# Performance work log

Hardware: AMD Instinct MI355X
Metric: run time of the kernel (lower is better)

Reference implementation:

```python
import jax, jax.numpy as jnp
import numpy as np

B, T, C = 2, 2048, 1024
H, D = 16, 64
EPS = 1e-6


def _layernorm(x, gamma, beta):
    # Faithful to the torch module: uses unbiased std (Bessel) and divides by (std + eps).
    mean = x.mean(-1, keepdims=True)
    std = jnp.sqrt(jnp.sum((x - mean) ** 2, axis=-1, keepdims=True) / (x.shape[-1] - 1))
    return gamma * (x - mean) / (std + EPS) + beta


def setup_inputs() -> dict:
    key = jax.random.key(0)
    ks = jax.random.split(key, 9)
    s = lambda fan_in: 1.0 / np.sqrt(fan_in)
    return {
        "x": jax.random.normal(ks[0], (B, T, C), dtype=jnp.float32),
        "qkv_w": jax.random.uniform(ks[1], (3 * C, C), jnp.float32, -s(C), s(C)),
        "proj_w": jax.random.uniform(ks[2], (C, C), jnp.float32, -s(C), s(C)),
        "proj_b": jax.random.uniform(ks[3], (C,), jnp.float32, -s(C), s(C)),
        "l1_w": jax.random.uniform(ks[4], (4 * C, C), jnp.float32, -s(C), s(C)),
        "l1_b": jax.random.uniform(ks[5], (4 * C,), jnp.float32, -s(C), s(C)),
        "l3_w": jax.random.uniform(ks[6], (C, 4 * C), jnp.float32, -s(4 * C), s(4 * C)),
        "l3_b": jax.random.uniform(ks[7], (C,), jnp.float32, -s(4 * C), s(4 * C)),
        "ln1_g": jnp.ones((C,), jnp.float32),
        "ln1_b": jnp.zeros((C,), jnp.float32),
        "ln2_g": jnp.ones((C,), jnp.float32),
        "ln2_b": jnp.zeros((C,), jnp.float32),
    }


def _attention(x, qkv_w, proj_w, proj_b):
    Bx, Tx, Cx = x.shape
    qkv = x @ qkv_w.T                      # [B,T,3C]
    q, k, v = jnp.split(qkv, 3, axis=-1)
    q = q.reshape(Bx, Tx, H, D)
    k = k.reshape(Bx, Tx, H, D)
    v = v.reshape(Bx, Tx, H, D)
    scores = jnp.einsum("bthd,bshd->bhts", q, k) * (D ** -0.5)  # [B,H,T,T]
    causal = jnp.tril(jnp.ones((Tx, Tx), dtype=bool))
    scores = jnp.where(causal, scores, -jnp.inf)
    attn = jax.nn.softmax(scores, axis=-1)
    out = jnp.einsum("bhts,bshd->bthd", attn, v).reshape(Bx, Tx, Cx)
    return out @ proj_w.T + proj_b


def _mlp(x, l1_w, l1_b, l3_w, l3_b):
    h = jax.nn.relu(x @ l1_w.T + l1_b)     # [B,T,4C]
    return h @ l3_w.T + l3_b


def reference(x, qkv_w, proj_w, proj_b, l1_w, l1_b, l3_w, l3_b, ln1_g, ln1_b, ln2_g, ln2_b):
    # Dropout is identity in eval mode.
    x1 = x + _attention(_layernorm(x, ln1_g, ln1_b), qkv_w, proj_w, proj_b)
    x2 = x1 + _mlp(_layernorm(x1, ln2_g, ln2_b), l1_w, l1_b, l3_w, l3_b)
    return x2
```

## Files before the change

kernel.cpp:

```cpp
#include <hip/hip_runtime.h>

typedef unsigned short u16;
typedef short short8 __attribute__((ext_vector_type(8)));
typedef float floatx4 __attribute__((ext_vector_type(4)));

#define TT 2048
#define CC 1024
#define QSCALE 0.1803368801111244f
#define MFIX 32.0f

__device__ __forceinline__ u16 f2bf(float f) {
  return (u16)((__float_as_uint(f) + 0x8000u) >> 16);
}

__device__ __forceinline__ unsigned int pk2bf(float a, float b) {
  unsigned int ua = __float_as_uint(a) + 0x8000u;
  unsigned int ub = __float_as_uint(b) + 0x8000u;
  return __builtin_amdgcn_perm(ub, ua, 0x07060302u);
}

__device__ __forceinline__ void glds16(const u16* g, u16* l) {
  __builtin_amdgcn_global_load_lds((const __attribute__((address_space(1))) void*)g,
                                   (__attribute__((address_space(3))) void*)l, 16, 0, 0);
}

__device__ __forceinline__ void ln_body(const float* __restrict__ x,
                                        const float* __restrict__ g,
                                        const float* __restrict__ b,
                                        u16* __restrict__ out, int row, int tid) {
  const float4* xr = (const float4*)(x + (size_t)row * CC);
  float4 v = xr[tid];
  float s = v.x + v.y + v.z + v.w;
  float sq = v.x * v.x + v.y * v.y + v.z * v.z + v.w * v.w;
#pragma unroll
  for (int off = 1; off < 64; off <<= 1) {
    s += __shfl_xor(s, off);
    sq += __shfl_xor(sq, off);
  }
  __shared__ float ss[4], ssq[4];
  int wave = tid >> 6;
  if ((tid & 63) == 0) { ss[wave] = s; ssq[wave] = sq; }
  __syncthreads();
  s = ss[0] + ss[1] + ss[2] + ss[3];
  sq = ssq[0] + ssq[1] + ssq[2] + ssq[3];
  float mean = s * (1.0f / CC);
  float var = (sq - (float)CC * mean * mean) * (1.0f / (CC - 1));
  float inv = 1.0f / (sqrtf(fmaxf(var, 0.0f)) + 1e-6f);
  float4 gv = ((const float4*)g)[tid];
  float4 bv = ((const float4*)b)[tid];
  ushort4 o;
  o.x = f2bf(gv.x * (v.x - mean) * inv + bv.x);
  o.y = f2bf(gv.y * (v.y - mean) * inv + bv.y);
  o.z = f2bf(gv.z * (v.z - mean) * inv + bv.z);
  o.w = f2bf(gv.w * (v.w - mean) * inv + bv.w);
  ((ushort4*)(out + (size_t)row * CC))[tid] = o;
}

__global__ __launch_bounds__(256) void cvt_ln_kernel(const float* __restrict__ w0,
                                                     const float* __restrict__ w1,
                                                     const float* __restrict__ w2,
                                                     const float* __restrict__ w3,
                                                     const float* __restrict__ x,
                                                     const float* __restrict__ lg,
                                                     const float* __restrict__ lb,
                                                     u16* __restrict__ o0,
                                                     u16* __restrict__ o1,
                                                     u16* __restrict__ o2,
                                                     u16* __restrict__ o3,
                                                     u16* __restrict__ oln) {
  int blk = blockIdx.x;
  if (blk >= 12288) {
    ln_body(x, lg, lb, oln, blk - 12288, threadIdx.x);
    return;
  }
  const float* in;
  u16* out;
  int base;
  if (blk < 3072)      { in = w0; out = o0; base = 0; }
  else if (blk < 4096) { in = w1; out = o1; base = 3072; }
  else if (blk < 8192) { in = w2; out = o2; base = 4096; }
  else                 { in = w3; out = o3; base = 8192; }
  int i = (blk - base) * 256 + threadIdx.x;
  float4 v = ((const float4*)in)[i];
  ushort4 o;
  o.x = f2bf(v.x); o.y = f2bf(v.y); o.z = f2bf(v.z); o.w = f2bf(v.w);
  ((ushort4*)out)[i] = o;
}

__global__ __launch_bounds__(256) void ln_kernel(const float* __restrict__ x,
                                                 const float* __restrict__ g,
                                                 const float* __restrict__ b,
                                                 u16* __restrict__ out) {
  ln_body(x, g, b, out, blockIdx.x, threadIdx.x);
}


#define STGP(st, g_)                                                      \
  glds16(gsrc + (size_t)(st) * 32 + (size_t)(g_) * 16 * K,                \
         &lds[(st) & 3][ldst + (g_) * 512])

#define BODY(t, VM)                                                       \
  {                                                                       \
    asm volatile("s_waitcnt vmcnt(" #VM ")" ::: "memory");                \
    __builtin_amdgcn_s_barrier();                                         \
    asm volatile("" ::: "memory");                                        \
    const u16* Ls = &lds[(t) & 3][0];                                     \
    bool stg_ = (t) + 3 < nst;                                            \
    if (stg_) {                                                           \
      _Pragma("unroll") for (int g_ = 0; g_ < GPP; g_++) STGP((t) + 3, g_); \
    }                                                                     \
    short8 bf[NJ];                                                        \
    _Pragma("unroll") for (int j_ = 0; j_ < NJ; j_++)                     \
        bf[j_] = *(const short8*)(Ls + bOff[j_]);                         \
    short8 a0_ = *(const short8*)(Ls + aOff[0]);                          \
    short8 a1_ = *(const short8*)(Ls + aOff[1]);                          \
    __builtin_amdgcn_s_setprio(1);                                        \
    _Pragma("unroll") for (int j_ = 0; j_ < NJ; j_++)                     \
        acc[0][j_] = __builtin_amdgcn_mfma_f32_16x16x32_bf16(a0_, bf[j_], acc[0][j_], 0, 0, 0); \
    _Pragma("unroll") for (int j_ = 0; j_ < NJ; j_++)                     \
        acc[1][j_] = __builtin_amdgcn_mfma_f32_16x16x32_bf16(a1_, bf[j_], acc[1][j_], 0, 0, 0); \
    __builtin_amdgcn_s_setprio(0);                                        \
    _Pragma("unroll") for (int ph_ = 1; ph_ < NPH; ph_++) {               \
      short8 c0_ = *(const short8*)(Ls + aOff[2 * ph_]);                  \
      short8 c1_ = *(const short8*)(Ls + aOff[2 * ph_ + 1]);              \
      if (stg_) {                                                         \
        _Pragma("unroll") for (int g_ = 0; g_ < GPP; g_++)                \
            STGP((t) + 3, ph_ * GPP + g_);                                \
      }                                                                   \
      __builtin_amdgcn_s_barrier();                                       \
      asm volatile("" ::: "memory");                                      \
      __builtin_amdgcn_s_setprio(1);                                      \
      _Pragma("unroll") for (int j_ = 0; j_ < NJ; j_++)                   \
          acc[2 * ph_][j_] = __builtin_amdgcn_mfma_f32_16x16x32_bf16(c0_, bf[j_], acc[2 * ph_][j_], 0, 0, 0); \
      _Pragma("unroll") for (int j_ = 0; j_ < NJ; j_++)                   \
          acc[2 * ph_ + 1][j_] = __builtin_amdgcn_mfma_f32_16x16x32_bf16(c1_, bf[j_], acc[2 * ph_ + 1][j_], 0, 0, 0); \
      __builtin_amdgcn_s_setprio(0);                                      \
    }                                                                     \
  }

template <int BM, int BN, int NWM, int NWN, int MODE>
__global__ __launch_bounds__(64 * NWM * NWN, 2) void gemmp(
    const u16* __restrict__ A, const u16* __restrict__ W,
    const float* __restrict__ bias, const float* __restrict__ resid,
    float* __restrict__ outf, u16* __restrict__ outb,
    int M, int N, int K) {
  constexpr int NW = NWM * NWN;
  constexpr int MI = BM / NWM / 16;
  constexpr int NJ = BN / NWN / 16;
  constexpr int ROWS = BM + BN;
  constexpr int NPH = MI / 2;
  constexpr int GPP = 4 / NPH;
  static_assert(ROWS / NW == 64, "each wave stages 64 rows");
  __shared__ u16 lds[4][ROWS * 32];

  const int tid = threadIdx.x;
  const int w = tid >> 6, lane = tid & 63;
  const int l15 = lane & 15, quad = lane >> 4;
  const int wm = (w / NWN) * (MI * 16);
  const int wn = (w % NWN) * (NJ * 16);
  const int tm = blockIdx.x * BM, tn = blockIdx.y * BN;

  const int srow = lane >> 2;
  const int xk = (lane & 3) ^ ((lane >> 4) & 3);
  const int wrow = w * 64;
  const u16* rowbase = (wrow < BM) ? (A + (size_t)(tm + wrow) * K)
                                   : (W + (size_t)(tn + wrow - BM) * K);
  const u16* gsrc = rowbase + (size_t)srow * K + xk * 8;
  const int ldst = wrow * 32;

  const int rx = (l15 >> 2) & 3;
  int aOff[MI], bOff[NJ];
#pragma unroll
  for (int m = 0; m < MI; m++) aOff[m] = (wm + m * 16 + l15) * 32 + ((quad ^ rx) * 8);
#pragma unroll
  for (int j = 0; j < NJ; j++) bOff[j] = (BM + wn + j * 16 + l15) * 32 + ((quad ^ rx) * 8);

  floatx4 acc[MI][NJ];
#pragma unroll
  for (int m = 0; m < MI; m++)
#pragma unroll
    for (int j = 0; j < NJ; j++) acc[m][j] = (floatx4){0.f, 0.f, 0.f, 0.f};

  const int nst = K >> 5;

#pragma unroll
  for (int st = 0; st < 3; st++)
#pragma unroll
    for (int g = 0; g < 4; g++) STGP(st, g);

#pragma unroll 4
  for (int t = 0; t < nst - 2; ++t) BODY(t, 8);
  BODY(nst - 2, 4);
  BODY(nst - 1, 0);

  float bb[NJ];
#pragma unroll
  for (int j = 0; j < NJ; j++)
    bb[j] = (MODE == 1 || MODE == 2) ? bias[tn + wn + j * 16 + l15] : 0.0f;
#pragma unroll
  for (int m = 0; m < MI; m++) {
    int row0 = tm + wm + m * 16 + quad * 4;
#pragma unroll
    for (int j = 0; j < NJ; j++) {
      int col = tn + wn + j * 16 + l15;
#pragma unroll
      for (int r = 0; r < 4; r++) {
        float v = acc[m][j][r];
        size_t idx = (size_t)(row0 + r) * N + col;
        if (MODE == 0) {
          if (col < 1024) v *= QSCALE;
          outb[idx] = f2bf(v);
        } else if (MODE == 1) {
          outf[idx] = v + bb[j] + resid[idx];
        } else {
          outb[idx] = f2bf(fmaxf(v + bb[j], 0.0f));
        }
      }
    }
  }
}

#undef STGP
#undef BODY

__global__ __launch_bounds__(256) void flash_kernel(const u16* __restrict__ qkv,
                                                    u16* __restrict__ attn) {
  int bid = blockIdx.x;
  int qt = 31 - (bid >> 5);
  int bh = bid & 31;
  int b = bh >> 4, h = bh & 15;
  int tid = threadIdx.x, w = tid >> 6, lane = tid & 63;
  int l15 = lane & 15, quad = lane >> 4;

  __shared__ u16 k_lds[128 * 64];
  __shared__ u16 vt_lds[64 * 136];
  __shared__ u16 p_lds[4][16 * 136];

  int qbase = qt * 64 + w * 16;
  const u16* qp = qkv + (size_t)(b * TT + qbase + l15) * 3072 + h * 64;
  short8 qf0 = *(const short8*)(qp + quad * 8);
  short8 qf1 = *(const short8*)(qp + 32 + quad * 8);

  float l_i = 0.0f;
  floatx4 accO[4];
#pragma unroll
  for (int jf = 0; jf < 4; jf++) accO[jf] = (floatx4){0.f, 0.f, 0.f, 0.f};

  int rsub = lane >> 3;
  int cg = (lane & 7) ^ rsub;
  const u16* Kg = qkv + (size_t)(b * TT + w * 32 + rsub) * 3072 + 1024 + h * 64 + cg * 8;
  u16* kL = k_lds + w * 32 * 64;
  int s4 = (tid & 31) * 4;
  int dg = (tid >> 5) * 8;
  const u16* Vg = qkv + (size_t)(b * TT + s4) * 3072 + 2048 + h * 64 + dg;

  int x = l15 & 7;
  int kOff[8];
#pragma unroll
  for (int i = 0; i < 8; i++) kOff[i] = (i * 16 + l15) * 64 + ((quad ^ x) * 8);
  int pRd = l15 * 136 + quad * 8;

  int nt = (qt + 2) >> 1;
  for (int kt = 0; kt < nt; kt++) {
    int s0 = kt * 128;
    size_t soff = (size_t)s0 * 3072;
    uint4 R0 = *(const uint4*)(Vg + soff);
    uint4 R1 = *(const uint4*)(Vg + soff + 3072);
    uint4 R2 = *(const uint4*)(Vg + soff + 6144);
    uint4 R3 = *(const uint4*)(Vg + soff + 9216);
    __syncthreads();
#pragma unroll
    for (int is = 0; is < 4; is++) glds16(Kg + soff + (size_t)is * 8 * 3072, kL + is * 512);
    {
      unsigned int a0[4] = {R0.x, R0.y, R0.z, R0.w};
      unsigned int a1[4] = {R1.x, R1.y, R1.z, R1.w};
      unsigned int a2[4] = {R2.x, R2.y, R2.z, R2.w};
      unsigned int a3[4] = {R3.x, R3.y, R3.z, R3.w};
#pragma unroll
      for (int p = 0; p < 4; p++) {
        uint2 ev, od;
        ev.x = __builtin_amdgcn_perm(a1[p], a0[p], 0x05040100u);
        ev.y = __builtin_amdgcn_perm(a3[p], a2[p], 0x05040100u);
        od.x = __builtin_amdgcn_perm(a1[p], a0[p], 0x07060302u);
        od.y = __builtin_amdgcn_perm(a3[p], a2[p], 0x07060302u);
        *(uint2*)(vt_lds + (dg + 2 * p) * 136 + s4) = ev;
        *(uint2*)(vt_lds + (dg + 2 * p + 1) * 136 + s4) = od;
      }
    }
    __syncthreads();

    floatx4 st[8];
#pragma unroll
    for (int i = 0; i < 8; i++) st[i] = (floatx4){0.f, 0.f, 0.f, 0.f};
#pragma unroll
    for (int i = 0; i < 8; i++) {
      short8 kf0 = *(const short8*)(k_lds + kOff[i]);
      short8 kf1 = *(const short8*)(k_lds + (kOff[i] ^ 32));
      st[i] = __builtin_amdgcn_mfma_f32_16x16x32_bf16(kf0, qf0, st[i], 0, 0, 0);
      st[i] = __builtin_amdgcn_mfma_f32_16x16x32_bf16(kf1, qf1, st[i], 0, 0, 0);
    }

    if (s0 + 127 > qbase) {
      int mg = qbase + l15;
#pragma unroll
      for (int i = 0; i < 8; i++)
#pragma unroll
        for (int r = 0; r < 4; r++) {
          int s = s0 + i * 16 + quad * 4 + r;
          if (s > mg) st[i][r] = -3.0e38f;
        }
    }

    float ts = 0.0f;
#pragma unroll
    for (int i = 0; i < 8; i++)
#pragma unroll
      for (int r = 0; r < 4; r++) {
        float p = __builtin_amdgcn_exp2f(st[i][r] - MFIX);
        st[i][r] = p;
        ts += p;
      }
    ts += __shfl_xor(ts, 16);
    ts += __shfl_xor(ts, 32);
    l_i += ts;

#pragma unroll
    for (int i = 0; i < 8; i++) {
      uint2 pk;
      pk.x = pk2bf(st[i][0], st[i][1]);
      pk.y = pk2bf(st[i][2], st[i][3]);
      *(uint2*)(p_lds[w] + l15 * 136 + i * 16 + quad * 4) = pk;
    }

    short8 pf[4];
#pragma unroll
    for (int c = 0; c < 4; c++) pf[c] = *(const short8*)(p_lds[w] + pRd + c * 32);
#pragma unroll
    for (int jf = 0; jf < 4; jf++) {
      int vOff = (jf * 16 + l15) * 136 + quad * 8;
#pragma unroll
      for (int c = 0; c < 4; c++) {
        short8 vf = *(const short8*)(vt_lds + vOff + c * 32);
        accO[jf] = __builtin_amdgcn_mfma_f32_16x16x32_bf16(pf[c], vf, accO[jf], 0, 0, 0);
      }
    }
  }

  float invl = 1.0f / l_i;
  float iR[4];
#pragma unroll
  for (int r = 0; r < 4; r++) iR[r] = __shfl(invl, quad * 4 + r);
  int orow = b * TT + qbase + quad * 4;
#pragma unroll
  for (int r = 0; r < 4; r++) {
    u16* op = attn + (size_t)(orow + r) * CC + h * 64 + l15;
#pragma unroll
    for (int jf = 0; jf < 4; jf++) op[jf * 16] = f2bf(accO[jf][r] * iR[r]);
  }
}

extern "C" void kernel_launch(void* const* d_in, const int* in_sizes, int n_in,
                              void* d_out, int out_size, void* d_ws, size_t ws_size,
                              hipStream_t stream) {
  const float* x      = (const float*)d_in[0];
  const float* qkv_w  = (const float*)d_in[1];
  const float* proj_w = (const float*)d_in[2];
  const float* proj_b = (const float*)d_in[3];
  const float* l1_w   = (const float*)d_in[4];
  const float* l1_b   = (const float*)d_in[5];
  const float* l3_w   = (const float*)d_in[6];
  const float* l3_b   = (const float*)d_in[7];
  const float* ln1_g  = (const float*)d_in[8];
  const float* ln1_b  = (const float*)d_in[9];
  const float* ln2_g  = (const float*)d_in[10];
  const float* ln2_b  = (const float*)d_in[11];
  float* out = (float*)d_out;
  char* ws = (char*)d_ws;

  u16* w_qkv  = (u16*)(ws + 0);
  u16* w_proj = (u16*)(ws + 6291456);
  u16* w_l1   = (u16*)(ws + 8388608);
  u16* w_l3   = (u16*)(ws + 16777216);
  u16* lnb    = (u16*)(ws + 25165824);
  u16* qkvb   = (u16*)(ws + 33554432);
  u16* attnb  = (u16*)(ws + 58720256);
  float* x1   = (float*)(ws + 67108864);
  u16* hb     = (u16*)(ws + 83886080);

  cvt_ln_kernel<<<16384, 256, 0, stream>>>(qkv_w, proj_w, l1_w, l3_w, x, ln1_g, ln1_b,
                                           w_qkv, w_proj, w_l1, w_l3, lnb);
  gemmp<256, 256, 2, 4, 0><<<dim3(16, 12), 512, 0, stream>>>(
      lnb, w_qkv, nullptr, nullptr, nullptr, qkvb, 4096, 3072, 1024);
  flash_kernel<<<1024, 256, 0, stream>>>(qkvb, attnb);
  gemmp<128, 128, 2, 2, 1><<<dim3(32, 8), 256, 0, stream>>>(
      attnb, w_proj, proj_b, x, x1, nullptr, 4096, 1024, 1024);
  ln_kernel<<<4096, 256, 0, stream>>>(x1, ln2_g, ln2_b, lnb);
  gemmp<256, 256, 2, 4, 2><<<dim3(16, 16), 512, 0, stream>>>(
      lnb, w_l1, l1_b, nullptr, nullptr, hb, 4096, 4096, 1024);
  gemmp<128, 128, 2, 2, 1><<<dim3(32, 8), 256, 0, stream>>>(
      hb, w_l3, l3_b, x1, out, nullptr, 4096, 1024, 4096);
}
```

Measured before the change: 312.8 us.

## Restructure GEMM pipeline to double-buffered BK=64 with 8-way swizzle

Replaces the 4-stage, BK=32 global-to-LDS pipeline with a 2-stage double buffer over BK=64 slices, using a new 8-chunk XOR swizzle and per-wave chunk assignment. Each K step now waits for all outstanding loads and issues fewer barriers per element of K, trading prefetch depth for fewer loop iterations and larger LDS tiles. The two N=1024 output GEMMs also switch to 128x64 tiles with twice as many blocks, to fill more compute units. The risk is exposed load latency, because only one stage is prefetched ahead and every iteration drains vmcnt to zero.

```diff
diff --git a/kernel.cpp b/kernel.cpp
--- a/kernel.cpp
+++ b/kernel.cpp
@@ -95,46 +95,35 @@
 }
 
 
-#define STGP(st, g_)                                                      \
-  glds16(gsrc + (size_t)(st) * 32 + (size_t)(g_) * 16 * K,                \
-         &lds[(st) & 3][ldst + (g_) * 512])
-
-#define BODY(t, VM)                                                       \
+#define STAGE(tt)                                                         \
   {                                                                       \
-    asm volatile("s_waitcnt vmcnt(" #VM ")" ::: "memory");                \
+    _Pragma("unroll") for (int g_ = 0; g_ < G; g_++)                      \
+        glds16(gptr[g_] + (size_t)(tt) * 64, &lds[(tt) & 1][ldd[g_]]);    \
+  }
+
+#define BODY(t)                                                           \
+  {                                                                       \
+    asm volatile("s_waitcnt vmcnt(0)" ::: "memory");                      \
     __builtin_amdgcn_s_barrier();                                         \
     asm volatile("" ::: "memory");                                        \
-    const u16* Ls = &lds[(t) & 3][0];                                     \
-    bool stg_ = (t) + 3 < nst;                                            \
-    if (stg_) {                                                           \
-      _Pragma("unroll") for (int g_ = 0; g_ < GPP; g_++) STGP((t) + 3, g_); \
-    }                                                                     \
-    short8 bf[NJ];                                                        \
-    _Pragma("unroll") for (int j_ = 0; j_ < NJ; j_++)                     \
-        bf[j_] = *(const short8*)(Ls + bOff[j_]);                         \
-    short8 a0_ = *(const short8*)(Ls + aOff[0]);                          \
-    short8 a1_ = *(const short8*)(Ls + aOff[1]);                          \
-    __builtin_amdgcn_s_setprio(1);                                        \
-    _Pragma("unroll") for (int j_ = 0; j_ < NJ; j_++)                     \
-        acc[0][j_] = __builtin_amdgcn_mfma_f32_16x16x32_bf16(a0_, bf[j_], acc[0][j_], 0, 0, 0); \
-    _Pragma("unroll") for (int j_ = 0; j_ < NJ; j_++)                     \
-        acc[1][j_] = __builtin_amdgcn_mfma_f32_16x16x32_bf16(a1_, bf[j_], acc[1][j_], 0, 0, 0); \
-    __builtin_amdgcn_s_setprio(0);                                        \
-    _Pragma("unroll") for (int ph_ = 1; ph_ < NPH; ph_++) {               \
-      short8 c0_ = *(const short8*)(Ls + aOff[2 * ph_]);                  \
-      short8 c1_ = *(const short8*)(Ls + aOff[2 * ph_ + 1]);              \
-      if (stg_) {                                                         \
-        _Pragma("unroll") for (int g_ = 0; g_ < GPP; g_++)                \
-            STGP((t) + 3, ph_ * GPP + g_);                                \
+    if ((t) + 1 < nst) STAGE((t) + 1);                                    \
+    const u16* Ls = &lds[(t) & 1][0];                                     \
+    _Pragma("unroll") for (int s_ = 0; s_ < 2; s_++) {                    \
+      short8 bf[NJ];                                                      \
+      _Pragma("unroll") for (int j_ = 0; j_ < NJ; j_++)                   \
+          bf[j_] = *(const short8*)(Ls + (bOff[j_] ^ (s_ << 5)));         \
+      _Pragma("unroll") for (int h_ = 0; h_ < MH; h_++) {                 \
+        short8 af[MC];                                                    \
+        _Pragma("unroll") for (int m_ = 0; m_ < MC; m_++)                 \
+            af[m_] = *(const short8*)(Ls + (aOff[h_ * MC + m_] ^ (s_ << 5))); \
+        if (s_ + h_ > 0) __builtin_amdgcn_s_barrier();                    \
+        __builtin_amdgcn_s_setprio(1);                                    \
+        _Pragma("unroll") for (int m_ = 0; m_ < MC; m_++)                 \
+            _Pragma("unroll") for (int j_ = 0; j_ < NJ; j_++)             \
+                acc[h_ * MC + m_][j_] = __builtin_amdgcn_mfma_f32_16x16x32_bf16( \
+                    af[m_], bf[j_], acc[h_ * MC + m_][j_], 0, 0, 0);      \
+        __builtin_amdgcn_s_setprio(0);                                    \
       }                                                                   \
-      __builtin_amdgcn_s_barrier();                                       \
-      asm volatile("" ::: "memory");                                      \
-      __builtin_amdgcn_s_setprio(1);                                      \
-      _Pragma("unroll") for (int j_ = 0; j_ < NJ; j_++)                   \
-          acc[2 * ph_][j_] = __builtin_amdgcn_mfma_f32_16x16x32_bf16(c0_, bf[j_], acc[2 * ph_][j_], 0, 0, 0); \
-      _Pragma("unroll") for (int j_ = 0; j_ < NJ; j_++)                   \
-          acc[2 * ph_ + 1][j_] = __builtin_amdgcn_mfma_f32_16x16x32_bf16(c1_, bf[j_], acc[2 * ph_ + 1][j_], 0, 0, 0); \
-      __builtin_amdgcn_s_setprio(0);                                      \
     }                                                                     \
   }
 
@@ -148,10 +137,11 @@
   constexpr int MI = BM / NWM / 16;
   constexpr int NJ = BN / NWN / 16;
   constexpr int ROWS = BM + BN;
-  constexpr int NPH = MI / 2;
-  constexpr int GPP = 4 / NPH;
-  static_assert(ROWS / NW == 64, "each wave stages 64 rows");
-  __shared__ u16 lds[4][ROWS * 32];
+  constexpr int G = ROWS / 8 / NW;
+  constexpr int MH = (MI > 4) ? 2 : 1;
+  constexpr int MC = MI / MH;
+  static_assert(ROWS % (8 * NW) == 0, "chunk assignment");
+  __shared__ u16 lds[2][ROWS * 64];
 
   const int tid = threadIdx.x;
   const int w = tid >> 6, lane = tid & 63;
@@ -160,20 +150,26 @@
   const int wn = (w % NWN) * (NJ * 16);
   const int tm = blockIdx.x * BM, tn = blockIdx.y * BN;
 
-  const int srow = lane >> 2;
-  const int xk = (lane & 3) ^ ((lane >> 4) & 3);
-  const int wrow = w * 64;
-  const u16* rowbase = (wrow < BM) ? (A + (size_t)(tm + wrow) * K)
-                                   : (W + (size_t)(tn + wrow - BM) * K);
-  const u16* gsrc = rowbase + (size_t)srow * K + xk * 8;
-  const int ldst = wrow * 32;
-
-  const int rx = (l15 >> 2) & 3;
+  const int srow = lane >> 3;
+  const int xk = (lane & 7) ^ srow;
+  const u16* gptr[G];
+  int ldd[G];
+#pragma unroll
+  for (int g = 0; g < G; g++) {
+    int c8 = (g * NW + w) * 8;
+    const u16* rb = (c8 < BM) ? (A + (size_t)(tm + c8) * K)
+                              : (W + (size_t)(tn + c8 - BM) * K);
+    gptr[g] = rb + (size_t)srow * K + xk * 8;
+    ldd[g] = c8 * 64;
+  }
+
   int aOff[MI], bOff[NJ];
 #pragma unroll
-  for (int m = 0; m < MI; m++) aOff[m] = (wm + m * 16 + l15) * 32 + ((quad ^ rx) * 8);
-#pragma unroll
-  for (int j = 0; j < NJ; j++) bOff[j] = (BM + wn + j * 16 + l15) * 32 + ((quad ^ rx) * 8);
+  for (int m = 0; m < MI; m++)
+    aOff[m] = (wm + m * 16 + l15) * 64 + ((quad ^ (l15 & 7)) * 8);
+#pragma unroll
+  for (int j = 0; j < NJ; j++)
+    bOff[j] = (BM + wn + j * 16 + l15) * 64 + ((quad ^ (l15 & 7)) * 8);
 
   floatx4 acc[MI][NJ];
 #pragma unroll
@@ -181,17 +177,12 @@
 #pragma unroll
     for (int j = 0; j < NJ; j++) acc[m][j] = (floatx4){0.f, 0.f, 0.f, 0.f};
 
-  const int nst = K >> 5;
-
-#pragma unroll
-  for (int st = 0; st < 3; st++)
-#pragma unroll
-    for (int g = 0; g < 4; g++) STGP(st, g);
-
-#pragma unroll 4
-  for (int t = 0; t < nst - 2; ++t) BODY(t, 8);
-  BODY(nst - 2, 4);
-  BODY(nst - 1, 0);
+  const int nst = K >> 6;
+
+  STAGE(0);
+
+#pragma unroll 2
+  for (int t = 0; t < nst; ++t) BODY(t);
 
   float bb[NJ];
 #pragma unroll
@@ -220,7 +211,7 @@
   }
 }
 
-#undef STGP
+#undef STAGE
 #undef BODY
 
 __global__ __launch_bounds__(256) void flash_kernel(const u16* __restrict__ qkv,
@@ -392,11 +383,11 @@
   gemmp<256, 256, 2, 4, 0><<<dim3(16, 12), 512, 0, stream>>>(
       lnb, w_qkv, nullptr, nullptr, nullptr, qkvb, 4096, 3072, 1024);
   flash_kernel<<<1024, 256, 0, stream>>>(qkvb, attnb);
-  gemmp<128, 128, 2, 2, 1><<<dim3(32, 8), 256, 0, stream>>>(
+  gemmp<128, 64, 2, 2, 1><<<dim3(32, 16), 256, 0, stream>>>(
       attnb, w_proj, proj_b, x, x1, nullptr, 4096, 1024, 1024);
   ln_kernel<<<4096, 256, 0, stream>>>(x1, ln2_g, ln2_b, lnb);
   gemmp<256, 256, 2, 4, 2><<<dim3(16, 16), 512, 0, stream>>>(
       lnb, w_l1, l1_b, nullptr, nullptr, hb, 4096, 4096, 1024);
-  gemmp<128, 128, 2, 2, 1><<<dim3(32, 8), 256, 0, stream>>>(
+  gemmp<128, 64, 2, 2, 1><<<dim3(32, 16), 256, 0, stream>>>(
       hb, w_l3, l3_b, x1, out, nullptr, 4096, 1024, 4096);
 }
```

After: 288.5 us. 7.8% less time.
